# Performance work log

Hardware: AMD Instinct MI355X
Metric: run time of the kernel (lower is better)

## Reference

```python
import jax, jax.numpy as jnp
import numpy as np

D_MODEL, D_STATE, EXPAND = 1024, 16, 2
D_INNER = EXPAND * D_MODEL
BATCH, SEQ = 4, 4096


def setup_inputs() -> dict:
    key = jax.random.key(0)
    ks = jax.random.split(key, 9)
    s = 0.02
    return {
        "x": jax.random.normal(ks[0], (BATCH, SEQ, D_MODEL), jnp.float32),
        # torch Linear weight [out,in] stored transposed here as [in,out]
        "W_in": jax.random.normal(ks[1], (D_MODEL, 2 * D_INNER), jnp.float32) * s,
        "conv_w": jax.random.normal(ks[2], (D_INNER, 1, 3), jnp.float32) * s,  # depthwise, groups=D_INNER
        "conv_b": jax.random.normal(ks[3], (D_INNER,), jnp.float32) * s,
        "W_B": jax.random.normal(ks[4], (D_INNER, D_STATE), jnp.float32) * s,
        "W_C": jax.random.normal(ks[5], (D_INNER, D_STATE), jnp.float32) * s,
        "A": jax.random.normal(ks[6], (D_STATE,), jnp.float32),
        "D": jnp.ones((D_INNER,), jnp.float32),
        "W_out": jax.random.normal(ks[7], (D_INNER, D_MODEL), jnp.float32) * s,
    }


def reference(x, W_in, conv_w, conv_b, W_B, W_C, A, D, W_out):
    d_inner = conv_w.shape[0]
    # input projection and split into main / residual gate paths
    xr = jnp.einsum("bld,de->ble", x, W_in)  # [B, L, 2*d_inner]
    x_main, res = xr[..., :d_inner], xr[..., d_inner:]
    # depthwise conv1d along seq (kernel 3, pad 1)
    xc = jax.lax.conv_general_dilated(
        x_main.transpose(0, 2, 1), conv_w, (1,), [(1, 1)],
        dimension_numbers=("NCH", "OIH", "NCH"), feature_group_count=d_inner)
    xc = (xc + conv_b[None, :, None]).transpose(0, 2, 1)  # [B, L, d_inner]
    xc = jax.nn.silu(xc)
    # selective-scan inputs
    Bt = jnp.einsum("bli,is->bls", xc, W_B)  # [B, L, d_state]
    Ct = jnp.einsum("bli,is->bls", xc, W_C)
    decay = jnp.exp(-jax.nn.softplus(A))  # exp(A_diag), [d_state]

    def step(state, bc):
        b_t, c_t = bc
        state = state * decay + b_t  # i=0: zeros*decay + B[0] == B[0]
        return state, jnp.sum(state * c_t, axis=-1)  # scalar per batch

    _, ys = jax.lax.scan(step, jnp.zeros_like(Bt[:, 0]),
                         (Bt.transpose(1, 0, 2), Ct.transpose(1, 0, 2)))
    ys = ys.T  # [B, L]
    y = ys[..., None] + xc * D  # broadcast scan output across d_inner
    y = y * jax.nn.silu(res)
    return jnp.einsum("bli,id->bld", y, W_out)
```

## Files before the change

### kernel.cpp

```cpp
#include <hip/hip_runtime.h>


typedef _Float16 half8 __attribute__((ext_vector_type(8)));
typedef float floatx4 __attribute__((ext_vector_type(4)));

#define D_MODEL 1024
#define D_INNER 2048
#define SEQ     4096
#define NBATCH  4
#define NROWS   (NBATCH * SEQ)
#define CHUNK   16
#define NCHUNK  (SEQ / CHUNK)
#define NTASK   (NBATCH * NCHUNK)

__device__ __forceinline__ void async16(_Float16* lds, const _Float16* g) {
    __builtin_amdgcn_global_load_lds((const __attribute__((address_space(1))) void*)g,
                                     (__attribute__((address_space(3))) void*)lds, 16, 0, 0);
}

__device__ __forceinline__ float siluf(float x) {
    return x / (1.f + __expf(-x));
}

__device__ __forceinline__ float decay_of(const float* A, int s) {
    return __expf(-log1pf(__expf(A[s])));
}


__global__ __launch_bounds__(256) void convert_f32_f16(const float* __restrict__ src,
                                                       _Float16* __restrict__ dst) {
    size_t idx = ((size_t)blockIdx.x * 256 + threadIdx.x) * 8;
    float4 a = *(const float4*)(src + idx);
    float4 b = *(const float4*)(src + idx + 4);
    half8 o = {(_Float16)a.x, (_Float16)a.y, (_Float16)a.z, (_Float16)a.w,
               (_Float16)b.x, (_Float16)b.y, (_Float16)b.z, (_Float16)b.w};
    *(half8*)(dst + idx) = o;
}

__global__ __launch_bounds__(256) void transpose_to_f16(const float* __restrict__ src,
                                                        _Float16* __restrict__ dst,
                                                        int K, int N) {
    __shared__ float tile[32][33];
    int n0 = blockIdx.x * 32, k0 = blockIdx.y * 32;
    int x = threadIdx.x, y = threadIdx.y;
#pragma unroll
    for (int r = 0; r < 32; r += 8)
        tile[y + r][x] = src[(size_t)(k0 + y + r) * N + (n0 + x)];
    __syncthreads();
#pragma unroll
    for (int r = 0; r < 32; r += 8)
        dst[(size_t)(n0 + y + r) * K + (k0 + x)] = (_Float16)tile[x][y + r];
}

__global__ __launch_bounds__(256) void convert_wbct(const float* __restrict__ WB,
                                                    const float* __restrict__ WC,
                                                    _Float16* __restrict__ WBCT) {
    int idx = blockIdx.x * 256 + threadIdx.x;
    int n = idx >> 11, k = idx & 2047;
    float v = (n < 16) ? WB[k * 16 + n] : WC[k * 16 + (n - 16)];
    WBCT[idx] = (_Float16)v;
}

__global__ __launch_bounds__(256) void zero_f32(float* __restrict__ p) {
    size_t idx = ((size_t)blockIdx.x * 256 + threadIdx.x) * 4;
    float4 z = {0.f, 0.f, 0.f, 0.f};
    *(float4*)(p + idx) = z;
}

template <typename OutT>
__global__ __launch_bounds__(256) void gemm_tn(const _Float16* __restrict__ A,
                                               const _Float16* __restrict__ BT,
                                               OutT* __restrict__ C,
                                               int M, int N, int K) {
    __shared__ __align__(16) _Float16 As[128 * 64];
    __shared__ __align__(16) _Float16 Bs[128 * 64];
    const int tid = threadIdx.x;
    const int wid = tid >> 6, lane = tid & 63;
    const int row0 = blockIdx.y * 128, col0 = blockIdx.x * 128;
    const int wm = (wid & 1) * 64, wn = (wid >> 1) * 64;

    floatx4 acc[4][4] = {};

    const int sr = lane >> 3;
    const int sc = ((lane & 7) ^ sr) * 8;
    const size_t aBase = (size_t)(row0 + wid * 32 + sr) * K + sc;
    const size_t bBase = (size_t)(col0 + wid * 32 + sr) * K + sc;
    _Float16* ldsA = As + wid * 2048;
    _Float16* ldsB = Bs + wid * 2048;

    const int fr = lane & 15, q = lane >> 4;
    const int frq = fr & 7;

    for (int k0 = 0; k0 < K; k0 += 64) {
        __syncthreads();
#pragma unroll
        for (int t = 0; t < 4; t++) {
            async16(ldsA + t * 512, A + aBase + (size_t)(t * 8) * K + k0);
            async16(ldsB + t * 512, BT + bBase + (size_t)(t * 8) * K + k0);
        }
        __syncthreads();
#pragma unroll
        for (int kk = 0; kk < 2; kk++) {
            const int sw = (((kk << 2) + q) ^ frq) * 8;
            half8 af[4], bf[4];
#pragma unroll
            for (int i = 0; i < 4; i++) {
                af[i] = *(const half8*)(As + (wm + i * 16 + fr) * 64 + sw);
                bf[i] = *(const half8*)(Bs + (wn + i * 16 + fr) * 64 + sw);
            }
#pragma unroll
            for (int i = 0; i < 4; i++)
#pragma unroll
                for (int j = 0; j < 4; j++)
                    acc[i][j] = __builtin_amdgcn_mfma_f32_16x16x32_f16(af[i], bf[j], acc[i][j], 0, 0, 0);
        }
    }

    const int er = (lane >> 4) * 4, ec = lane & 15;
#pragma unroll
    for (int i = 0; i < 4; i++)
#pragma unroll
        for (int j = 0; j < 4; j++)
#pragma unroll
            for (int r = 0; r < 4; r++) {
                int row = row0 + wm + i * 16 + er + r;
                int col = col0 + wn + j * 16 + ec;
                C[(size_t)row * N + col] = (OutT)acc[i][j][r];
            }
}

__global__ __launch_bounds__(256) void bc_gemm(const _Float16* __restrict__ A,
                                               const _Float16* __restrict__ BT,
                                               float* __restrict__ C) {
    const int K = D_INNER;
    __shared__ __align__(16) _Float16 As[64 * 64];
    __shared__ __align__(16) _Float16 Bs[32 * 64];
    const int tid = threadIdx.x, wid = tid >> 6, lane = tid & 63;
    const int row0 = blockIdx.x * 64;
    const int kbeg = blockIdx.y * (K / 2), kend = kbeg + K / 2;
    floatx4 acc[2] = {};

    const int srow = lane >> 3;
    const int scol = (lane & 7) * 8;
    const size_t aOff0 = (size_t)(row0 + wid * 16 + srow) * K + scol;
    const size_t aOff1 = aOff0 + (size_t)8 * K;
    const size_t bOff  = (size_t)(wid * 8 + srow) * K + scol;
    _Float16* ldsA = As + wid * 1024;
    _Float16* ldsB = Bs + wid * 512;
    const int fr = lane & 15, fc = (lane >> 4) * 8;

    for (int k0 = kbeg; k0 < kend; k0 += 64) {
        __syncthreads();
        async16(ldsA,       A + aOff0 + k0);
        async16(ldsA + 512, A + aOff1 + k0);
        async16(ldsB,       BT + bOff + k0);
        __syncthreads();
#pragma unroll
        for (int s = 0; s < 2; s++) {
            half8 af = *(const half8*)(As + (wid * 16 + fr) * 64 + s * 32 + fc);
#pragma unroll
            for (int nj = 0; nj < 2; nj++) {
                half8 bf = *(const half8*)(Bs + (nj * 16 + fr) * 64 + s * 32 + fc);
                acc[nj] = __builtin_amdgcn_mfma_f32_16x16x32_f16(af, bf, acc[nj], 0, 0, 0);
            }
        }
    }
    const int er = (lane >> 4) * 4, ec = lane & 15;
#pragma unroll
    for (int nj = 0; nj < 2; nj++)
#pragma unroll
        for (int r = 0; r < 4; r++)
            atomicAdd(&C[(size_t)(row0 + wid * 16 + er + r) * 32 + nj * 16 + ec], acc[nj][r]);
}

__global__ __launch_bounds__(256) void conv_silu_chunk(const _Float16* __restrict__ xr,
                                                       const float* __restrict__ cw,
                                                       const float* __restrict__ cb,
                                                       _Float16* __restrict__ xc) {
    const int task = blockIdx.x;
    const int c = task & (NCHUNK - 1);
    const int row0 = (task >> 8) * SEQ + c * CHUNK;
    const int col0 = threadIdx.x * 8;

    float w0[8], w1[8], w2[8], bb[8];
#pragma unroll
    for (int j = 0; j < 8; j++) {
        w0[j] = cw[(col0 + j) * 3];
        w1[j] = cw[(col0 + j) * 3 + 1];
        w2[j] = cw[(col0 + j) * 3 + 2];
        bb[j] = cb[col0 + j];
    }
    half8 prev = {}, cur, next;
    if (c > 0) prev = *(const half8*)(xr + (size_t)(row0 - 1) * 4096 + col0);
    cur = *(const half8*)(xr + (size_t)row0 * 4096 + col0);
#pragma unroll
    for (int r = 0; r < CHUNK; r++) {
        if (c == NCHUNK - 1 && r == CHUNK - 1) {
            half8 z = {};
            next = z;
        } else {
            next = *(const half8*)(xr + (size_t)(row0 + r + 1) * 4096 + col0);
        }
        half8 o;
#pragma unroll
        for (int j = 0; j < 8; j++) {
            float a = (float)prev[j] * w0[j] + (float)cur[j] * w1[j] +
                      (float)next[j] * w2[j] + bb[j];
            o[j] = (_Float16)siluf(a);
        }
        *(half8*)(xc + (size_t)(row0 + r) * D_INNER + col0) = o;
        prev = cur;
        cur = next;
    }
}


__global__ __launch_bounds__(256) void scan_p1(const float* __restrict__ BtCt,
                                               const float* __restrict__ A,
                                               float* __restrict__ fin) {
    int g = blockIdx.x * 256 + threadIdx.x;
    int task = g >> 4, s = g & 15;
    int b = task >> 8, c = task & (NCHUNK - 1);
    const float decay = decay_of(A, s);
    size_t r = ((size_t)b * SEQ + c * CHUNK) * 32;
    float st = 0.f;
#pragma unroll
    for (int j = 0; j < CHUNK; j++)
        st = st * decay + BtCt[r + (size_t)j * 32 + s];
    fin[task * 16 + s] = st;
}

__global__ __launch_bounds__(64) void scan_p2(const float* __restrict__ fin,
                                              const float* __restrict__ A,
                                              float* __restrict__ carry) {
    int t = threadIdx.x;
    int b = t >> 4, s = t & 15;
    float decay = decay_of(A, s);
    float d16 = decay;
#pragma unroll
    for (int k = 0; k < 4; k++) d16 *= d16;
    float cy = 0.f;
#pragma unroll 8
    for (int c = 0; c < NCHUNK; c++) {
        int idx = ((b * NCHUNK) + c) * 16 + s;
        carry[idx] = cy;
        cy = cy * d16 + fin[idx];
    }
}

__global__ __launch_bounds__(256) void scan_p3_fuse(const float* __restrict__ BtCt,
                                                    const float* __restrict__ A,
                                                    const float* __restrict__ carry,
                                                    const float* __restrict__ D,
                                                    const _Float16* __restrict__ xr,
                                                    _Float16* __restrict__ xc) {
    __shared__ float ysl[CHUNK];
    const int task = blockIdx.x;
    const int b = task >> 8, c = task & (NCHUNK - 1);
    const int row0 = b * SEQ + c * CHUNK;
    const int tid = threadIdx.x;

    if (tid < 16) {
        const int s = tid;
        const float decay = decay_of(A, s);
        size_t r = (size_t)row0 * 32;
        float bt[CHUNK], ct[CHUNK];
#pragma unroll
        for (int j = 0; j < CHUNK; j++) {
            bt[j] = BtCt[r + (size_t)j * 32 + s];
            ct[j] = BtCt[r + (size_t)j * 32 + 16 + s];
        }
        float st = carry[task * 16 + s];
        float yv[CHUNK];
#pragma unroll
        for (int j = 0; j < CHUNK; j++) {
            st = st * decay + bt[j];
            yv[j] = st * ct[j];
        }
#pragma unroll
        for (int j = 0; j < CHUNK; j++) {
            float y = yv[j];
            y += __shfl_xor(y, 1, 16);
            y += __shfl_xor(y, 2, 16);
            y += __shfl_xor(y, 4, 16);
            y += __shfl_xor(y, 8, 16);
            if (s == 0) ysl[j] = y;
        }
    }
    __syncthreads();

#pragma unroll
    for (int it = 0; it < 16; it++) {
        int chunk = it * 256 + tid;
        int rl = chunk >> 8;
        int colb = (chunk & 255) * 8;
        size_t row = (size_t)(row0 + rl);
        float yv = ysl[rl];
        half8 x8 = *(const half8*)(xc + row * D_INNER + colb);
        half8 r8 = *(const half8*)(xr + row * 4096 + 2048 + colb);
        float4 d0 = *(const float4*)(D + colb);
        float4 d1 = *(const float4*)(D + colb + 4);
        half8 o;
        float dd[8] = {d0.x, d0.y, d0.z, d0.w, d1.x, d1.y, d1.z, d1.w};
#pragma unroll
        for (int j = 0; j < 8; j++) {
            float y = yv + (float)x8[j] * dd[j];
            o[j] = (_Float16)(y * siluf((float)r8[j]));
        }
        *(half8*)(xc + row * D_INNER + colb) = o;
    }
}

extern "C" void kernel_launch(void* const* d_in, const int* in_sizes, int n_in,
                              void* d_out, int out_size, void* d_ws, size_t ws_size,
                              hipStream_t stream) {
    const float* x      = (const float*)d_in[0];
    const float* W_in   = (const float*)d_in[1];
    const float* conv_w = (const float*)d_in[2];
    const float* conv_b = (const float*)d_in[3];
    const float* W_B    = (const float*)d_in[4];
    const float* W_C    = (const float*)d_in[5];
    const float* A      = (const float*)d_in[6];
    const float* D      = (const float*)d_in[7];
    const float* W_out  = (const float*)d_in[8];
    float* out = (float*)d_out;

    char* ws = (char*)d_ws;
    size_t off = 0;
    auto alloc = [&](size_t bytes) { size_t o = off; off += (bytes + 255) & ~(size_t)255; return o; };
    _Float16* xh    = (_Float16*)(ws + alloc((size_t)NROWS * D_MODEL * 2));
    _Float16* WinT  = (_Float16*)(ws + alloc((size_t)4096 * 1024 * 2));
    _Float16* WoutT = (_Float16*)(ws + alloc((size_t)1024 * 2048 * 2));
    _Float16* WBCT  = (_Float16*)(ws + alloc((size_t)32 * 2048 * 2));
    _Float16* xr    = (_Float16*)(ws + alloc((size_t)NROWS * 4096 * 2));
    _Float16* xc    = (_Float16*)(ws + alloc((size_t)NROWS * D_INNER * 2));
    float*    BtCt  = (float*)(ws + alloc((size_t)NROWS * 32 * 4));
    float*    fin   = (float*)(ws + alloc((size_t)NTASK * 16 * 4));
    float*    carry = (float*)(ws + alloc((size_t)NTASK * 16 * 4));

    convert_f32_f16<<<(NROWS * D_MODEL) / (256 * 8), 256, 0, stream>>>(x, xh);
    transpose_to_f16<<<dim3(4096 / 32, 1024 / 32), dim3(32, 8), 0, stream>>>(W_in, WinT, 1024, 4096);
    transpose_to_f16<<<dim3(1024 / 32, 2048 / 32), dim3(32, 8), 0, stream>>>(W_out, WoutT, 2048, 1024);
    convert_wbct<<<(32 * 2048) / 256, 256, 0, stream>>>(W_B, W_C, WBCT);
    zero_f32<<<(NROWS * 32) / (256 * 4), 256, 0, stream>>>(BtCt);
    gemm_tn<_Float16><<<dim3(4096 / 128, NROWS / 128), 256, 0, stream>>>(xh, WinT, xr, NROWS, 4096, 1024);
    conv_silu_chunk<<<NTASK, 256, 0, stream>>>(xr, conv_w, conv_b, xc);
    bc_gemm<<<dim3(NROWS / 64, 2), 256, 0, stream>>>(xc, WBCT, BtCt);
    scan_p1<<<NTASK * 16 / 256, 256, 0, stream>>>(BtCt, A, fin);
    scan_p2<<<1, 64, 0, stream>>>(fin, A, carry);
    scan_p3_fuse<<<NTASK, 256, 0, stream>>>(BtCt, A, carry, D, xr, xc);
    gemm_tn<float><<<dim3(1024 / 128, NROWS / 128), 256, 0, stream>>>(xc, WoutT, out, NROWS, 1024, 2048);
}
```

Baseline: 508.2 us.

## Fuse conv+SiLU, B/C projection and chunk scan pass into one kernel

Merges the depthwise conv+SiLU, the B/C projection GEMM and the first scan pass into a single kernel. Each block computes 32 rows of xc, stages them in LDS and runs MFMA against WBCT read straight from global memory. It then reduces the per-wave partials in LDS and writes BtCt and the chunk-final states directly. This removes the zeroing kernel, the atomics, the xc re-read by the separate GEMM, and several launches. The input-projection GEMM is also split into two half-size launches, which only adds a launch and has no clear benefit.

```diff
diff --git a/kernel.cpp b/kernel.cpp
--- a/kernel.cpp
+++ b/kernel.cpp
@@ -59,12 +59,6 @@
     int n = idx >> 11, k = idx & 2047;
     float v = (n < 16) ? WB[k * 16 + n] : WC[k * 16 + (n - 16)];
     WBCT[idx] = (_Float16)v;
-}
-
-__global__ __launch_bounds__(256) void zero_f32(float* __restrict__ p) {
-    size_t idx = ((size_t)blockIdx.x * 256 + threadIdx.x) * 4;
-    float4 z = {0.f, 0.f, 0.f, 0.f};
-    *(float4*)(p + idx) = z;
 }
 
 template <typename OutT>
@@ -129,105 +123,110 @@
             }
 }
 
-__global__ __launch_bounds__(256) void bc_gemm(const _Float16* __restrict__ A,
-                                               const _Float16* __restrict__ BT,
-                                               float* __restrict__ C) {
-    const int K = D_INNER;
-    __shared__ __align__(16) _Float16 As[64 * 64];
-    __shared__ __align__(16) _Float16 Bs[32 * 64];
+__global__ __launch_bounds__(256) void conv_bc_fin(const _Float16* __restrict__ xr,
+                                                   const float* __restrict__ cw,
+                                                   const float* __restrict__ cb,
+                                                   const _Float16* __restrict__ WBCT,
+                                                   const float* __restrict__ A,
+                                                   _Float16* __restrict__ xc,
+                                                   float* __restrict__ BtCt,
+                                                   float* __restrict__ fin) {
+    __shared__ __align__(16) _Float16 As[4 * 32 * 128];
     const int tid = threadIdx.x, wid = tid >> 6, lane = tid & 63;
-    const int row0 = blockIdx.x * 64;
-    const int kbeg = blockIdx.y * (K / 2), kend = kbeg + K / 2;
-    floatx4 acc[2] = {};
-
-    const int srow = lane >> 3;
-    const int scol = (lane & 7) * 8;
-    const size_t aOff0 = (size_t)(row0 + wid * 16 + srow) * K + scol;
-    const size_t aOff1 = aOff0 + (size_t)8 * K;
-    const size_t bOff  = (size_t)(wid * 8 + srow) * K + scol;
-    _Float16* ldsA = As + wid * 1024;
-    _Float16* ldsB = Bs + wid * 512;
-    const int fr = lane & 15, fc = (lane >> 4) * 8;
-
-    for (int k0 = kbeg; k0 < kend; k0 += 64) {
-        __syncthreads();
-        async16(ldsA,       A + aOff0 + k0);
-        async16(ldsA + 512, A + aOff1 + k0);
-        async16(ldsB,       BT + bOff + k0);
-        __syncthreads();
-#pragma unroll
-        for (int s = 0; s < 2; s++) {
-            half8 af = *(const half8*)(As + (wid * 16 + fr) * 64 + s * 32 + fc);
-#pragma unroll
-            for (int nj = 0; nj < 2; nj++) {
-                half8 bf = *(const half8*)(Bs + (nj * 16 + fr) * 64 + s * 32 + fc);
-                acc[nj] = __builtin_amdgcn_mfma_f32_16x16x32_f16(af, bf, acc[nj], 0, 0, 0);
+    const int row0 = blockIdx.x * 32;
+    const int l0 = row0 & (SEQ - 1);
+    const int cg = lane & 15;
+    const int rg = lane >> 4;
+    const int fr = lane & 15, q = lane >> 4;
+    _Float16* As_w = As + wid * 4096;
+    const int r0 = rg * 8;
+
+    floatx4 acc[2][2] = {};
+
+    for (int t = 0; t < 4; t++) {
+        const int kbase = wid * 512 + t * 128;
+        const int gcol = kbase + cg * 8;
+        float w0[8], w1[8], w2[8], bb[8];
+#pragma unroll
+        for (int j = 0; j < 8; j++) {
+            w0[j] = cw[(gcol + j) * 3];
+            w1[j] = cw[(gcol + j) * 3 + 1];
+            w2[j] = cw[(gcol + j) * 3 + 2];
+            bb[j] = cb[gcol + j];
+        }
+        half8 prev = {}, cur, nxt;
+        if (!(l0 == 0 && rg == 0))
+            prev = *(const half8*)(xr + (size_t)(row0 + r0 - 1) * 4096 + gcol);
+        cur = *(const half8*)(xr + (size_t)(row0 + r0) * 4096 + gcol);
+#pragma unroll
+        for (int r = 0; r < 8; r++) {
+            if (r == 7 && rg == 3 && l0 + 32 == SEQ) {
+                half8 z = {};
+                nxt = z;
+            } else {
+                nxt = *(const half8*)(xr + (size_t)(row0 + r0 + r + 1) * 4096 + gcol);
             }
-        }
-    }
+            half8 o;
+#pragma unroll
+            for (int j = 0; j < 8; j++) {
+                float a = (float)prev[j] * w0[j] + (float)cur[j] * w1[j] +
+                          (float)nxt[j] * w2[j] + bb[j];
+                o[j] = (_Float16)siluf(a);
+            }
+            const int lrow = r0 + r;
+            *(half8*)(xc + (size_t)(row0 + lrow) * D_INNER + gcol) = o;
+            *(half8*)(As_w + lrow * 128 + ((cg ^ (lrow & 7)) * 8)) = o;
+            prev = cur;
+            cur = nxt;
+        }
+#pragma unroll
+        for (int ks = 0; ks < 4; ks++) {
+            half8 af[2], bf[2];
+#pragma unroll
+            for (int rt = 0; rt < 2; rt++)
+                af[rt] = *(const half8*)(As_w + (rt * 16 + fr) * 128 +
+                                         (((ks * 4 + q) ^ (fr & 7)) * 8));
+#pragma unroll
+            for (int ot = 0; ot < 2; ot++)
+                bf[ot] = *(const half8*)(WBCT + (size_t)(ot * 16 + fr) * D_INNER +
+                                         kbase + ks * 32 + q * 8);
+#pragma unroll
+            for (int rt = 0; rt < 2; rt++)
+#pragma unroll
+                for (int ot = 0; ot < 2; ot++)
+                    acc[rt][ot] = __builtin_amdgcn_mfma_f32_16x16x32_f16(af[rt], bf[ot], acc[rt][ot], 0, 0, 0);
+        }
+    }
+
+    __syncthreads();
+    float* red = (float*)As;
+    float* btl = (float*)As + 4096;
     const int er = (lane >> 4) * 4, ec = lane & 15;
 #pragma unroll
-    for (int nj = 0; nj < 2; nj++)
-#pragma unroll
-        for (int r = 0; r < 4; r++)
-            atomicAdd(&C[(size_t)(row0 + wid * 16 + er + r) * 32 + nj * 16 + ec], acc[nj][r]);
-}
-
-__global__ __launch_bounds__(256) void conv_silu_chunk(const _Float16* __restrict__ xr,
-                                                       const float* __restrict__ cw,
-                                                       const float* __restrict__ cb,
-                                                       _Float16* __restrict__ xc) {
-    const int task = blockIdx.x;
-    const int c = task & (NCHUNK - 1);
-    const int row0 = (task >> 8) * SEQ + c * CHUNK;
-    const int col0 = threadIdx.x * 8;
-
-    float w0[8], w1[8], w2[8], bb[8];
-#pragma unroll
-    for (int j = 0; j < 8; j++) {
-        w0[j] = cw[(col0 + j) * 3];
-        w1[j] = cw[(col0 + j) * 3 + 1];
-        w2[j] = cw[(col0 + j) * 3 + 2];
-        bb[j] = cb[col0 + j];
-    }
-    half8 prev = {}, cur, next;
-    if (c > 0) prev = *(const half8*)(xr + (size_t)(row0 - 1) * 4096 + col0);
-    cur = *(const half8*)(xr + (size_t)row0 * 4096 + col0);
-#pragma unroll
-    for (int r = 0; r < CHUNK; r++) {
-        if (c == NCHUNK - 1 && r == CHUNK - 1) {
-            half8 z = {};
-            next = z;
-        } else {
-            next = *(const half8*)(xr + (size_t)(row0 + r + 1) * 4096 + col0);
-        }
-        half8 o;
-#pragma unroll
-        for (int j = 0; j < 8; j++) {
-            float a = (float)prev[j] * w0[j] + (float)cur[j] * w1[j] +
-                      (float)next[j] * w2[j] + bb[j];
-            o[j] = (_Float16)siluf(a);
-        }
-        *(half8*)(xc + (size_t)(row0 + r) * D_INNER + col0) = o;
-        prev = cur;
-        cur = next;
-    }
-}
-
-
-__global__ __launch_bounds__(256) void scan_p1(const float* __restrict__ BtCt,
-                                               const float* __restrict__ A,
-                                               float* __restrict__ fin) {
-    int g = blockIdx.x * 256 + threadIdx.x;
-    int task = g >> 4, s = g & 15;
-    int b = task >> 8, c = task & (NCHUNK - 1);
-    const float decay = decay_of(A, s);
-    size_t r = ((size_t)b * SEQ + c * CHUNK) * 32;
-    float st = 0.f;
-#pragma unroll
-    for (int j = 0; j < CHUNK; j++)
-        st = st * decay + BtCt[r + (size_t)j * 32 + s];
-    fin[task * 16 + s] = st;
+    for (int rt = 0; rt < 2; rt++)
+#pragma unroll
+        for (int ot = 0; ot < 2; ot++)
+#pragma unroll
+            for (int rr = 0; rr < 4; rr++)
+                red[wid * 1024 + (rt * 16 + er + rr) * 32 + ot * 16 + ec] = acc[rt][ot][rr];
+    __syncthreads();
+#pragma unroll
+    for (int i = 0; i < 4; i++) {
+        int idx = i * 256 + tid;
+        float v = red[idx] + red[1024 + idx] + red[2048 + idx] + red[3072 + idx];
+        btl[idx] = v;
+        BtCt[(size_t)row0 * 32 + idx] = v;
+    }
+    __syncthreads();
+    if (tid < 32) {
+        const int ch = tid >> 4, s = tid & 15;
+        const float decay = decay_of(A, s);
+        float st = 0.f;
+#pragma unroll
+        for (int r = 0; r < CHUNK; r++)
+            st = st * decay + btl[(ch * 16 + r) * 32 + s];
+        fin[((row0 >> 4) + ch) * 16 + s] = st;
+    }
 }
 
 __global__ __launch_bounds__(64) void scan_p2(const float* __restrict__ fin,
@@ -342,11 +341,10 @@
     transpose_to_f16<<<dim3(4096 / 32, 1024 / 32), dim3(32, 8), 0, stream>>>(W_in, WinT, 1024, 4096);
     transpose_to_f16<<<dim3(1024 / 32, 2048 / 32), dim3(32, 8), 0, stream>>>(W_out, WoutT, 2048, 1024);
     convert_wbct<<<(32 * 2048) / 256, 256, 0, stream>>>(W_B, W_C, WBCT);
-    zero_f32<<<(NROWS * 32) / (256 * 4), 256, 0, stream>>>(BtCt);
-    gemm_tn<_Float16><<<dim3(4096 / 128, NROWS / 128), 256, 0, stream>>>(xh, WinT, xr, NROWS, 4096, 1024);
-    conv_silu_chunk<<<NTASK, 256, 0, stream>>>(xr, conv_w, conv_b, xc);
-    bc_gemm<<<dim3(NROWS / 64, 2), 256, 0, stream>>>(xc, WBCT, BtCt);
-    scan_p1<<<NTASK * 16 / 256, 256, 0, stream>>>(BtCt, A, fin);
+    gemm_tn<_Float16><<<dim3(4096 / 128, 64), 256, 0, stream>>>(xh, WinT, xr, NROWS / 2, 4096, 1024);
+    gemm_tn<_Float16><<<dim3(4096 / 128, 64), 256, 0, stream>>>(xh + (size_t)8192 * 1024, WinT,
+                                                                xr + (size_t)8192 * 4096, NROWS / 2, 4096, 1024);
+    conv_bc_fin<<<NROWS / 32, 256, 0, stream>>>(xr, conv_w, conv_b, WBCT, A, xc, BtCt, fin);
     scan_p2<<<1, 64, 0, stream>>>(fin, A, carry);
     scan_p3_fuse<<<NTASK, 256, 0, stream>>>(BtCt, A, carry, D, xr, xc);
     gemm_tn<float><<<dim3(1024 / 128, NROWS / 128), 256, 0, stream>>>(xc, WoutT, out, NROWS, 1024, 2048);
```

Measured after the change: 501.6 us. About the same (-1.3%).
